# Performance work log

Measured on AMD Instinct MI355X. Metric: run time of the kernel, lower is better.

Reference implementation:

```python
import jax, jax.numpy as jnp
import numpy as np

DIM = 512
HEADS = 8


def setup_inputs() -> dict:
    key = jax.random.key(0)
    ks = jax.random.split(key, 9)
    s = 1.0 / np.sqrt(DIM)
    x = jax.random.normal(ks[0], (2, 4096, DIM), dtype=jnp.float32)
    Wq = jax.random.uniform(ks[1], (DIM, DIM), jnp.float32, -s, s)
    bq = jax.random.uniform(ks[2], (DIM,), jnp.float32, -s, s)
    Wk = jax.random.uniform(ks[3], (DIM, DIM), jnp.float32, -s, s)
    bk = jax.random.uniform(ks[4], (DIM,), jnp.float32, -s, s)
    Wv = jax.random.uniform(ks[5], (DIM, DIM), jnp.float32, -s, s)
    bv = jax.random.uniform(ks[6], (DIM,), jnp.float32, -s, s)
    Wo = jax.random.uniform(ks[7], (DIM, DIM), jnp.float32, -s, s)
    bo = jax.random.uniform(ks[8], (DIM,), jnp.float32, -s, s)
    return {"x": x, "Wq": Wq, "bq": bq, "Wk": Wk, "bk": bk,
            "Wv": Wv, "bv": bv, "Wo": Wo, "bo": bo}


def reference(x, Wq, bq, Wk, bk, Wv, bv, Wo, bo):
    b, t, d = x.shape
    h = HEADS
    dq = d // h
    scale = dq ** -0.5
    # projections: torch Linear is x @ W.T + b
    q = (x @ Wq.T + bq).reshape(b, t, h, dq)
    k = (x @ Wk.T + bk).reshape(b, t, h, dq)
    v = (x @ Wv.T + bv).reshape(b, t, h, dq)
    # attention scores [b, h, t, t] (full O(T^2) matrix, as in the original)
    att = jnp.einsum("bqhd,bkhd->bhqk", q, k) * scale
    att = jax.nn.softmax(att, axis=-1)
    out = jnp.einsum("bhqk,bkhd->bqhd", att, v).reshape(b, t, d)
    return out @ Wo.T + bo
```

## Files before the change

### kernel.cpp

```cpp
#include <hip/hip_runtime.h>

typedef short bf16x8 __attribute__((ext_vector_type(8)));
typedef float f32x4 __attribute__((ext_vector_type(4)));
typedef unsigned u32x2 __attribute__((ext_vector_type(2)));
typedef unsigned u32x4 __attribute__((ext_vector_type(4)));

#define MFMA(a, b, c) __builtin_amdgcn_mfma_f32_16x16x32_bf16((a), (b), (c), 0, 0, 0)

__device__ __forceinline__ unsigned cvtpk(float a, float b) {
    unsigned r;
    asm("v_cvt_pk_bf16_f32 %0, %1, %2" : "=v"(r) : "v"(a), "v"(b));
    return r;
}

__device__ __forceinline__ void gload16(const void* g, void* l) {
    __builtin_amdgcn_global_load_lds(
        (const __attribute__((address_space(1))) unsigned*)g,
        (__attribute__((address_space(3))) unsigned*)l, 16, 0, 0);
}

__global__ __launch_bounds__(256) void cvt_kernel(
    const float* __restrict__ x,
    const float* __restrict__ w0, const float* __restrict__ w1,
    const float* __restrict__ w2, const float* __restrict__ w3,
    unsigned short* __restrict__ xd,
    unsigned short* __restrict__ d0, unsigned short* __restrict__ d1,
    unsigned short* __restrict__ d2, unsigned short* __restrict__ d3)
{
    int bid = blockIdx.x;
    const float* src;
    unsigned short* dst;
    int off;
    if (bid < 4096) { src = x; dst = xd; off = bid; }
    else {
        int s = (bid - 4096) >> 8;
        src = s == 0 ? w0 : (s == 1 ? w1 : (s == 2 ? w2 : w3));
        dst = s == 0 ? d0 : (s == 1 ? d1 : (s == 2 ? d2 : d3));
        off = (bid - 4096) & 255;
    }
    size_t i = ((size_t)off * 256 + threadIdx.x) * 4;
    float4 v = *(const float4*)(src + i);
    uint2 pk;
    pk.x = cvtpk(v.x, v.y);
    pk.y = cvtpk(v.z, v.w);
    *(uint2*)(dst + i) = pk;
}

__device__ __forceinline__ void gemm128_core(
    const unsigned short* __restrict__ A, const unsigned short* __restrict__ W,
    int m0, int n0, int tid, unsigned short* sA, unsigned short* sB,
    f32x4 acc[4][4])
{
    const int lane = tid & 63, wid = tid >> 6;
    const int quad = lane >> 4, l15 = lane & 15;
    const int wm = wid >> 1, wn = wid & 1;

    const int gl_r = lane >> 3;
    const int gl_kc = (lane & 7) ^ gl_r;

    #pragma unroll
    for (int i = 0; i < 4; i++)
        #pragma unroll
        for (int j = 0; j < 4; j++) {
            f32x4 z = {0.f, 0.f, 0.f, 0.f};
            acc[i][j] = z;
        }

    for (int k0 = 0; k0 < 512; k0 += 64) {
        #pragma unroll
        for (int p = 0; p < 4; p++) {
            int chunk = wid * 4 + p;
            int row = chunk * 8 + gl_r;
            gload16(A + (size_t)(m0 + row) * 512 + k0 + gl_kc * 8,
                    (char*)sA + chunk * 1024);
            gload16(W + (size_t)(n0 + row) * 512 + k0 + gl_kc * 8,
                    (char*)sB + chunk * 1024);
        }
        __syncthreads();
        #pragma unroll
        for (int ks = 0; ks < 2; ks++) {
            bf16x8 af[4], bfr[4];
            #pragma unroll
            for (int i = 0; i < 4; i++) {
                int row = wm * 64 + i * 16 + l15;
                int kc = ks * 4 + quad;
                af[i] = *(const bf16x8*)((const char*)sA + row * 128 + ((kc ^ (row & 7)) << 4));
            }
            #pragma unroll
            for (int j = 0; j < 4; j++) {
                int row = wn * 64 + j * 16 + l15;
                int kc = ks * 4 + quad;
                bfr[j] = *(const bf16x8*)((const char*)sB + row * 128 + ((kc ^ (row & 7)) << 4));
            }
            #pragma unroll
            for (int i = 0; i < 4; i++)
                #pragma unroll
                for (int j = 0; j < 4; j++)
                    acc[i][j] = MFMA(af[i], bfr[j], acc[i][j]);
        }
        __syncthreads();
    }
}

__global__ __launch_bounds__(256) void qkv_kernel(
    const unsigned short* __restrict__ x,
    const unsigned short* __restrict__ Wq, const float* __restrict__ bq,
    const unsigned short* __restrict__ Wk, const float* __restrict__ bk,
    const unsigned short* __restrict__ Wv, const float* __restrict__ bv,
    unsigned short* __restrict__ qo, unsigned short* __restrict__ ko,
    unsigned short* __restrict__ vo)
{
    __shared__ unsigned short sA[128 * 64];
    __shared__ unsigned short sB[128 * 64];
    const int tid = threadIdx.x;
    const int by = blockIdx.y;
    const int sel = by >> 2;
    const int n0 = (by & 3) * 128;
    const int m0 = blockIdx.x * 128;
    const unsigned short* W = sel == 0 ? Wq : (sel == 1 ? Wk : Wv);
    const float* bias = sel == 0 ? bq : (sel == 1 ? bk : bv);

    f32x4 acc[4][4];
    gemm128_core(x, W, m0, n0, tid, sA, sB, acc);

    const int lane = tid & 63, wid = tid >> 6;
    const int quad = lane >> 4, l15 = lane & 15;
    const int wm = wid >> 1, wn = wid & 1;
    float bv4[4];
    #pragma unroll
    for (int j = 0; j < 4; j++) bv4[j] = bias[n0 + wn * 64 + j * 16 + l15];

    if (sel != 1) {
        const float SC = (sel == 0) ? 0.125f * 1.44269504088896f : 1.0f;
        unsigned short* dstT = (sel == 0) ? qo : vo;
        #pragma unroll
        for (int i = 0; i < 4; i++) {
            #pragma unroll
            for (int j = 0; j < 4; j++) {
                int n = n0 + wn * 64 + j * 16 + l15;
                int h = n >> 6, d = n & 63;
                int m = m0 + wm * 64 + i * 16 + quad * 4;
                int b = m >> 12, t = m & 4095;
                uint2 pk;
                pk.x = cvtpk((acc[i][j][0] + bv4[j]) * SC,
                             (acc[i][j][1] + bv4[j]) * SC);
                pk.y = cvtpk((acc[i][j][2] + bv4[j]) * SC,
                             (acc[i][j][3] + bv4[j]) * SC);
                *(uint2*)(dstT + ((size_t)(b * 8 + h) * 64 + d) * 4096 + t) = pk;
            }
        }
    } else {
        #pragma unroll
        for (int i = 0; i < 4; i++) {
            #pragma unroll
            for (int j = 0; j < 4; j++) {
                int n = n0 + wn * 64 + j * 16 + l15;
                int h = n >> 6, d = n & 63;
                int m = m0 + wm * 64 + i * 16 + quad * 4;
                int b = m >> 12, t = m & 4095;
                size_t base2 = ((size_t)(b * 8 + h) * 4096 + t) * 64 + d;
                unsigned p01 = cvtpk(acc[i][j][0] + bv4[j], acc[i][j][1] + bv4[j]);
                unsigned p23 = cvtpk(acc[i][j][2] + bv4[j], acc[i][j][3] + bv4[j]);
                ko[base2]       = (unsigned short)p01;
                ko[base2 + 64]  = (unsigned short)(p01 >> 16);
                ko[base2 + 128] = (unsigned short)p23;
                ko[base2 + 192] = (unsigned short)(p23 >> 16);
            }
        }
    }
}

__global__ __launch_bounds__(512, 4) void attn_kernel(
    const unsigned short* __restrict__ qg, const unsigned short* __restrict__ kg,
    const unsigned short* __restrict__ vtg, unsigned short* __restrict__ og)
{
    __shared__ unsigned char smem[66048];

    const int tid = threadIdx.x;
    const int lane = tid & 63;
    const int w = tid >> 6;
    const int g = tid >> 8;
    const int wg = w & 3;
    const int sw = w & 3;
    const int quad = lane >> 4, l15 = lane & 15;
    const int bh = blockIdx.y;
    const size_t base = (size_t)bh * 4096 * 64;
    const unsigned short* Q = qg + base;
    const unsigned short* K = kg + base;
    const unsigned short* VT = vtg + base;
    const int qt0 = blockIdx.x * 128;

    const int srow = lane >> 3;
    const int skc  = (lane & 7) ^ srow;

    int kLaneOff[2], vLaneOff[2], dKOff[2], dVOff[2];
    #pragma unroll
    for (int p = 0; p < 2; p++) {
        int chunk = wg * 2 + p;
        int row = chunk * 8 + srow;
        kLaneOff[p] = row * 64 + skc * 8;
        vLaneOff[p] = row * 4096 + skc * 8;
        dKOff[p] = g * 8192 + chunk * 1024;
        dVOff[p] = 16384 + g * 8192 + chunk * 1024;
    }

    int okS[4][2], okV[4][2];
    #pragma unroll
    for (int rb = 0; rb < 4; rb++)
        #pragma unroll
        for (int ks = 0; ks < 2; ks++) {
            int row = rb * 16 + l15;
            int kc = ks * 4 + quad;
            int sl = ((kc ^ (row & 7)) << 4);
            okS[rb][ks] = g * 8192 + row * 128 + sl;
            okV[rb][ks] = 16384 + g * 8192 + row * 128 + sl;
        }

    bf16x8 qf[2][2];
    #pragma unroll
    for (int cb = 0; cb < 2; cb++) {
        int t = qt0 + sw * 32 + cb * 16 + l15;
        #pragma unroll
        for (int ks = 0; ks < 2; ks++) {
            bf16x8 v;
            #pragma unroll
            for (int e = 0; e < 8; e++)
                v[e] = (short)Q[(size_t)(ks * 32 + quad * 8 + e) * 4096 + t];
            qf[cb][ks] = v;
        }
    }

    f32x4 ot[4][2];
    #pragma unroll
    for (int i = 0; i < 4; i++)
        #pragma unroll
        for (int cb = 0; cb < 2; cb++) {
            f32x4 z = {0.f, 0.f, 0.f, 0.f};
            ot[i][cb] = z;
        }
    f32x4 ls[2];
    {
        f32x4 z = {0.f, 0.f, 0.f, 0.f};
        ls[0] = z; ls[1] = z;
    }
    const short one_b = (short)0x3F80;
    const bf16x8 ones = {one_b, one_b, one_b, one_b, one_b, one_b, one_b, one_b};

    {
        int kb = g * 64;
        #pragma unroll
        for (int p = 0; p < 2; p++) {
            gload16(K + (size_t)kb * 64 + kLaneOff[p], smem + dKOff[p]);
            gload16(VT + (size_t)kb + vLaneOff[p], smem + dVOff[p]);
        }
    }

    auto do_iter = [&](int it, int bufoff) {
        __asm__ __volatile__("s_waitcnt vmcnt(0)" ::: "memory");
        __syncthreads();

        if (it < 31) {
            int kb = (2 * (it + 1) + g) * 64;
            int od = bufoff ^ 32768;
            #pragma unroll
            for (int p = 0; p < 2; p++) {
                gload16(K + (size_t)kb * 64 + kLaneOff[p], smem + od + dKOff[p]);
                gload16(VT + (size_t)kb + vLaneOff[p], smem + od + dVOff[p]);
            }
        }

        #pragma unroll
        for (int half = 0; half < 2; half++) {
            unsigned xA[2], yA[2], zB[2], wB[2];
            #pragma unroll
            for (int rb2 = 0; rb2 < 2; rb2++) {
                int rb = half * 2 + rb2;
                f32x4 s0 = {0.f, 0.f, 0.f, 0.f};
                f32x4 s1 = {0.f, 0.f, 0.f, 0.f};
                __builtin_amdgcn_s_setprio(1);
                #pragma unroll
                for (int ks = 0; ks < 2; ks++) {
                    bf16x8 ka = *(const bf16x8*)(smem + bufoff + okS[rb][ks]);
                    s0 = MFMA(ka, qf[0][ks], s0);
                    s1 = MFMA(ka, qf[1][ks], s1);
                }
                __builtin_amdgcn_s_setprio(0);
                unsigned e0 = cvtpk(__builtin_amdgcn_exp2f(s0[0]),
                                    __builtin_amdgcn_exp2f(s0[1]));
                unsigned e1 = cvtpk(__builtin_amdgcn_exp2f(s0[2]),
                                    __builtin_amdgcn_exp2f(s0[3]));
                unsigned f0 = cvtpk(__builtin_amdgcn_exp2f(s1[0]),
                                    __builtin_amdgcn_exp2f(s1[1]));
                unsigned f1 = cvtpk(__builtin_amdgcn_exp2f(s1[2]),
                                    __builtin_amdgcn_exp2f(s1[3]));
                if (rb2 == 0) { xA[0] = e0; yA[0] = e1; xA[1] = f0; yA[1] = f1; }
                else          { zB[0] = e0; wB[0] = e1; zB[1] = f0; wB[1] = f1; }
            }

            bf16x8 pf[2];
            #pragma unroll
            for (int cb = 0; cb < 2; cb++) {
                u32x2 s  = __builtin_amdgcn_permlane32_swap(xA[cb], zB[cb], false, false);
                u32x2 t  = __builtin_amdgcn_permlane16_swap(s[0], s[1], false, false);
                u32x2 s2 = __builtin_amdgcn_permlane32_swap(yA[cb], wB[cb], false, false);
                u32x2 t2 = __builtin_amdgcn_permlane16_swap(s2[0], s2[1], false, false);
                u32x4 fr = { t[0], t2[0], t[1], t2[1] };
                pf[cb] = __builtin_bit_cast(bf16x8, fr);
            }

            __builtin_amdgcn_s_setprio(1);
            ls[0] = MFMA(ones, pf[0], ls[0]);
            ls[1] = MFMA(ones, pf[1], ls[1]);
            #pragma unroll
            for (int rbd = 0; rbd < 4; rbd++) {
                bf16x8 vf = *(const bf16x8*)(smem + bufoff + okV[rbd][half]);
                ot[rbd][0] = MFMA(vf, pf[0], ot[rbd][0]);
                ot[rbd][1] = MFMA(vf, pf[1], ot[rbd][1]);
            }
            __builtin_amdgcn_s_setprio(0);
        }
    };

    for (int it2 = 0; it2 < 16; it2++) {
        do_iter(2 * it2, 0);
        do_iter(2 * it2 + 1, 32768);
    }

    float* oc = (float*)smem;
    float* lc = (float*)(smem + 65536);
    if (g == 1) {
        #pragma unroll
        for (int cb = 0; cb < 2; cb++) {
            int qb = sw * 32 + cb * 16 + l15;
            if (quad == 0) lc[qb] = ls[cb][0];
            #pragma unroll
            for (int rbd = 0; rbd < 4; rbd++) {
                int dc = rbd * 4 + quad;
                *(f32x4*)((char*)oc + qb * 256 + ((dc ^ (qb & 15)) << 4)) = ot[rbd][cb];
            }
        }
    }
    __syncthreads();
    if (g == 0) {
        const int b = bh >> 3, h = bh & 7;
        #pragma unroll
        for (int cb = 0; cb < 2; cb++) {
            int qb = sw * 32 + cb * 16 + l15;
            float inv = 1.f / (ls[cb][0] + lc[qb]);
            int q = qt0 + qb;
            #pragma unroll
            for (int rbd = 0; rbd < 4; rbd++) {
                int dc = rbd * 4 + quad;
                f32x4 o2 = *(const f32x4*)((char*)oc + qb * 256 + ((dc ^ (qb & 15)) << 4));
                uint2 pk;
                pk.x = cvtpk((ot[rbd][cb][0] + o2[0]) * inv,
                             (ot[rbd][cb][1] + o2[1]) * inv);
                pk.y = cvtpk((ot[rbd][cb][2] + o2[2]) * inv,
                             (ot[rbd][cb][3] + o2[3]) * inv);
                *(uint2*)(og + ((size_t)(b * 4096 + q) * 512 + h * 64 + rbd * 16 + quad * 4)) = pk;
            }
        }
    }
}

__global__ __launch_bounds__(256) void out_kernel(
    const unsigned short* __restrict__ attn,
    const unsigned short* __restrict__ Wo, const float* __restrict__ bo,
    float* __restrict__ out)
{
    __shared__ unsigned short sA[128 * 64];
    __shared__ unsigned short sB[128 * 64];
    const int tid = threadIdx.x;
    const int m0 = blockIdx.x * 128;
    const int n0 = blockIdx.y * 128;

    f32x4 acc[4][4];
    gemm128_core(attn, Wo, m0, n0, tid, sA, sB, acc);

    const int lane = tid & 63, wid = tid >> 6;
    const int quad = lane >> 4, l15 = lane & 15;
    const int wm = wid >> 1, wn = wid & 1;
    float bv4[4];
    #pragma unroll
    for (int j = 0; j < 4; j++) bv4[j] = bo[n0 + wn * 64 + j * 16 + l15];
    #pragma unroll
    for (int i = 0; i < 4; i++) {
        #pragma unroll
        for (int j = 0; j < 4; j++) {
            int n = n0 + wn * 64 + j * 16 + l15;
            #pragma unroll
            for (int r = 0; r < 4; r++) {
                int m = m0 + wm * 64 + i * 16 + quad * 4 + r;
                out[(size_t)m * 512 + n] = acc[i][j][r] + bv4[j];
            }
        }
    }
}

extern "C" void kernel_launch(void* const* d_in, const int* in_sizes, int n_in,
                              void* d_out, int out_size, void* d_ws, size_t ws_size,
                              hipStream_t stream) {
    const float* x  = (const float*)d_in[0];
    const float* Wq = (const float*)d_in[1];
    const float* bq = (const float*)d_in[2];
    const float* Wk = (const float*)d_in[3];
    const float* bk = (const float*)d_in[4];
    const float* Wv = (const float*)d_in[5];
    const float* bv = (const float*)d_in[6];
    const float* Wo = (const float*)d_in[7];
    const float* bo = (const float*)d_in[8];
    unsigned short* ws = (unsigned short*)d_ws;

    const size_t NTOK = (size_t)2 * 4096 * 512;
    const size_t WSZ = (size_t)512 * 512;
    unsigned short* xb  = ws;
    unsigned short* Wqb = ws + NTOK;
    unsigned short* Wkb = Wqb + WSZ;
    unsigned short* Wvb = Wkb + WSZ;
    unsigned short* Wob = Wvb + WSZ;
    unsigned short* q_ws = Wob + WSZ;
    unsigned short* k_ws = q_ws + NTOK;
    unsigned short* v_ws = k_ws + NTOK;
    unsigned short* a_ws = v_ws + NTOK;

    cvt_kernel<<<5120, 256, 0, stream>>>(x, Wq, Wk, Wv, Wo, xb, Wqb, Wkb, Wvb, Wob);
    qkv_kernel<<<dim3(64, 12), 256, 0, stream>>>(xb, Wqb, bq, Wkb, bk, Wvb, bv,
                                                 q_ws, k_ws, v_ws);
    attn_kernel<<<dim3(32, 16), 512, 0, stream>>>(q_ws, k_ws, v_ws, a_ws);
    out_kernel<<<dim3(64, 4), 256, 0, stream>>>(a_ws, Wob, bo,
                                                (float*)d_out);
}
```

Baseline: 190.5 us.

## Fuse fp32-to-bf16 conversion into GEMM tile loads, dropping cvt kernel

Removes the separate conversion kernel and instead has the QKV and output GEMMs load fp32 x and weights directly, converting to bf16 in registers before writing swizzled LDS tiles. This removes one launch and the write/read round trip of a bf16 copy of x and the weights. In exchange the GEMMs read twice as many bytes per tile, x is re-converted by each of the 12 column blocks, and the asynchronous global-to-LDS loads are replaced by register-staged loads, which can reduce load/compute overlap.

```diff
diff --git a/kernel.cpp b/kernel.cpp
--- a/kernel.cpp
+++ b/kernel.cpp
@@ -19,35 +19,19 @@
         (__attribute__((address_space(3))) unsigned*)l, 16, 0, 0);
 }
 
-__global__ __launch_bounds__(256) void cvt_kernel(
-    const float* __restrict__ x,
-    const float* __restrict__ w0, const float* __restrict__ w1,
-    const float* __restrict__ w2, const float* __restrict__ w3,
-    unsigned short* __restrict__ xd,
-    unsigned short* __restrict__ d0, unsigned short* __restrict__ d1,
-    unsigned short* __restrict__ d2, unsigned short* __restrict__ d3)
-{
-    int bid = blockIdx.x;
-    const float* src;
-    unsigned short* dst;
-    int off;
-    if (bid < 4096) { src = x; dst = xd; off = bid; }
-    else {
-        int s = (bid - 4096) >> 8;
-        src = s == 0 ? w0 : (s == 1 ? w1 : (s == 2 ? w2 : w3));
-        dst = s == 0 ? d0 : (s == 1 ? d1 : (s == 2 ? d2 : d3));
-        off = (bid - 4096) & 255;
-    }
-    size_t i = ((size_t)off * 256 + threadIdx.x) * 4;
-    float4 v = *(const float4*)(src + i);
-    uint2 pk;
-    pk.x = cvtpk(v.x, v.y);
-    pk.y = cvtpk(v.z, v.w);
-    *(uint2*)(dst + i) = pk;
-}
-
-__device__ __forceinline__ void gemm128_core(
-    const unsigned short* __restrict__ A, const unsigned short* __restrict__ W,
+__device__ __forceinline__ uint4 ld8f32_bf16(const float* src) {
+    float4 v0 = *(const float4*)(src);
+    float4 v1 = *(const float4*)(src + 4);
+    uint4 pk;
+    pk.x = cvtpk(v0.x, v0.y);
+    pk.y = cvtpk(v0.z, v0.w);
+    pk.z = cvtpk(v1.x, v1.y);
+    pk.w = cvtpk(v1.z, v1.w);
+    return pk;
+}
+
+__device__ __forceinline__ void gemm128_f32core(
+    const float* __restrict__ A, const float* __restrict__ W,
     int m0, int n0, int tid, unsigned short* sA, unsigned short* sB,
     f32x4 acc[4][4])
 {
@@ -55,9 +39,6 @@
     const int quad = lane >> 4, l15 = lane & 15;
     const int wm = wid >> 1, wn = wid & 1;
 
-    const int gl_r = lane >> 3;
-    const int gl_kc = (lane & 7) ^ gl_r;
-
     #pragma unroll
     for (int i = 0; i < 4; i++)
         #pragma unroll
@@ -69,12 +50,12 @@
     for (int k0 = 0; k0 < 512; k0 += 64) {
         #pragma unroll
         for (int p = 0; p < 4; p++) {
-            int chunk = wid * 4 + p;
-            int row = chunk * 8 + gl_r;
-            gload16(A + (size_t)(m0 + row) * 512 + k0 + gl_kc * 8,
-                    (char*)sA + chunk * 1024);
-            gload16(W + (size_t)(n0 + row) * 512 + k0 + gl_kc * 8,
-                    (char*)sB + chunk * 1024);
+            int c = tid + p * 256;
+            int row = c >> 3, kc = c & 7;
+            uint4 va = ld8f32_bf16(A + (size_t)(m0 + row) * 512 + k0 + kc * 8);
+            *(uint4*)((char*)sA + row * 128 + ((kc ^ (row & 7)) << 4)) = va;
+            uint4 vb = ld8f32_bf16(W + (size_t)(n0 + row) * 512 + k0 + kc * 8);
+            *(uint4*)((char*)sB + row * 128 + ((kc ^ (row & 7)) << 4)) = vb;
         }
         __syncthreads();
         #pragma unroll
@@ -103,10 +84,10 @@
 }
 
 __global__ __launch_bounds__(256) void qkv_kernel(
-    const unsigned short* __restrict__ x,
-    const unsigned short* __restrict__ Wq, const float* __restrict__ bq,
-    const unsigned short* __restrict__ Wk, const float* __restrict__ bk,
-    const unsigned short* __restrict__ Wv, const float* __restrict__ bv,
+    const float* __restrict__ x,
+    const float* __restrict__ Wq, const float* __restrict__ bq,
+    const float* __restrict__ Wk, const float* __restrict__ bk,
+    const float* __restrict__ Wv, const float* __restrict__ bv,
     unsigned short* __restrict__ qo, unsigned short* __restrict__ ko,
     unsigned short* __restrict__ vo)
 {
@@ -117,11 +98,11 @@
     const int sel = by >> 2;
     const int n0 = (by & 3) * 128;
     const int m0 = blockIdx.x * 128;
-    const unsigned short* W = sel == 0 ? Wq : (sel == 1 ? Wk : Wv);
+    const float* W = sel == 0 ? Wq : (sel == 1 ? Wk : Wv);
     const float* bias = sel == 0 ? bq : (sel == 1 ? bk : bv);
 
     f32x4 acc[4][4];
-    gemm128_core(x, W, m0, n0, tid, sA, sB, acc);
+    gemm128_f32core(x, W, m0, n0, tid, sA, sB, acc);
 
     const int lane = tid & 63, wid = tid >> 6;
     const int quad = lane >> 4, l15 = lane & 15;
@@ -365,7 +346,7 @@
 
 __global__ __launch_bounds__(256) void out_kernel(
     const unsigned short* __restrict__ attn,
-    const unsigned short* __restrict__ Wo, const float* __restrict__ bo,
+    const float* __restrict__ Wo, const float* __restrict__ bo,
     float* __restrict__ out)
 {
     __shared__ unsigned short sA[128 * 64];
@@ -374,12 +355,54 @@
     const int m0 = blockIdx.x * 128;
     const int n0 = blockIdx.y * 128;
 
-    f32x4 acc[4][4];
-    gemm128_core(attn, Wo, m0, n0, tid, sA, sB, acc);
-
     const int lane = tid & 63, wid = tid >> 6;
     const int quad = lane >> 4, l15 = lane & 15;
     const int wm = wid >> 1, wn = wid & 1;
+
+    f32x4 acc[4][4];
+    #pragma unroll
+    for (int i = 0; i < 4; i++)
+        #pragma unroll
+        for (int j = 0; j < 4; j++) {
+            f32x4 z = {0.f, 0.f, 0.f, 0.f};
+            acc[i][j] = z;
+        }
+
+    for (int k0 = 0; k0 < 512; k0 += 64) {
+        #pragma unroll
+        for (int p = 0; p < 4; p++) {
+            int c = tid + p * 256;
+            int row = c >> 3, kc = c & 7;
+            uint4 va = *(const uint4*)(attn + (size_t)(m0 + row) * 512 + k0 + kc * 8);
+            *(uint4*)((char*)sA + row * 128 + ((kc ^ (row & 7)) << 4)) = va;
+            uint4 vb = ld8f32_bf16(Wo + (size_t)(n0 + row) * 512 + k0 + kc * 8);
+            *(uint4*)((char*)sB + row * 128 + ((kc ^ (row & 7)) << 4)) = vb;
+        }
+        __syncthreads();
+        #pragma unroll
+        for (int ks = 0; ks < 2; ks++) {
+            bf16x8 af[4], bfr[4];
+            #pragma unroll
+            for (int i = 0; i < 4; i++) {
+                int row = wm * 64 + i * 16 + l15;
+                int kc = ks * 4 + quad;
+                af[i] = *(const bf16x8*)((const char*)sA + row * 128 + ((kc ^ (row & 7)) << 4));
+            }
+            #pragma unroll
+            for (int j = 0; j < 4; j++) {
+                int row = wn * 64 + j * 16 + l15;
+                int kc = ks * 4 + quad;
+                bfr[j] = *(const bf16x8*)((const char*)sB + row * 128 + ((kc ^ (row & 7)) << 4));
+            }
+            #pragma unroll
+            for (int i = 0; i < 4; i++)
+                #pragma unroll
+                for (int j = 0; j < 4; j++)
+                    acc[i][j] = MFMA(af[i], bfr[j], acc[i][j]);
+        }
+        __syncthreads();
+    }
+
     float bv4[4];
     #pragma unroll
     for (int j = 0; j < 4; j++) bv4[j] = bo[n0 + wn * 64 + j * 16 + l15];
@@ -412,21 +435,14 @@
     unsigned short* ws = (unsigned short*)d_ws;
 
     const size_t NTOK = (size_t)2 * 4096 * 512;
-    const size_t WSZ = (size_t)512 * 512;
-    unsigned short* xb  = ws;
-    unsigned short* Wqb = ws + NTOK;
-    unsigned short* Wkb = Wqb + WSZ;
-    unsigned short* Wvb = Wkb + WSZ;
-    unsigned short* Wob = Wvb + WSZ;
-    unsigned short* q_ws = Wob + WSZ;
+    unsigned short* q_ws = ws;
     unsigned short* k_ws = q_ws + NTOK;
     unsigned short* v_ws = k_ws + NTOK;
     unsigned short* a_ws = v_ws + NTOK;
 
-    cvt_kernel<<<5120, 256, 0, stream>>>(x, Wq, Wk, Wv, Wo, xb, Wqb, Wkb, Wvb, Wob);
-    qkv_kernel<<<dim3(64, 12), 256, 0, stream>>>(xb, Wqb, bq, Wkb, bk, Wvb, bv,
+    qkv_kernel<<<dim3(64, 12), 256, 0, stream>>>(x, Wq, bq, Wk, bk, Wv, bv,
                                                  q_ws, k_ws, v_ws);
     attn_kernel<<<dim3(32, 16), 512, 0, stream>>>(q_ws, k_ws, v_ws, a_ws);
-    out_kernel<<<dim3(64, 4), 256, 0, stream>>>(a_ws, Wob, bo,
+    out_kernel<<<dim3(64, 4), 256, 0, stream>>>(a_ws, Wo, bo,
                                                 (float*)d_out);
 }
```

Result: slower. 198.1 us (+4.0%).
